# Performance work log

Hardware: AMD Instinct MI355X
Metric: run time of the kernel (lower is better)

Reference implementation:

```python
import jax, jax.numpy as jnp
import numpy as np

CLIP_LIMIT = 4.0
GRID = (8, 8)
NBINS = 256
B, H, W = 8, 2048, 2048


def setup_inputs() -> dict:
    key = jax.random.key(0)
    img = jax.random.randint(key, (B, H, W), 0, 256).astype(jnp.float32)
    return {"image": img}


def _clahe(image):
    b, h, w = image.shape
    gy, gx = GRID
    th, tw = h // gy, w // gx
    area = th * tw
    # quantize to bins (indices are non-differentiable constants)
    bins = jnp.clip(jax.lax.stop_gradient(image), 0, 255).astype(jnp.int32)  # [B,H,W]

    # ---- per-tile 256-bin histograms via scatter-add ----
    tiles = bins.reshape(b, gy, th, gx, tw).transpose(0, 1, 3, 2, 4)
    tiles = tiles.reshape(b * gy * gx, area)                       # [ntiles, area]
    n = b * gy * gx
    hist = jnp.zeros((n, NBINS), jnp.int32).at[jnp.arange(n)[:, None], tiles].add(1)

    # ---- clip and redistribute excess (OpenCV semantics) ----
    clip_lim = max(int(CLIP_LIMIT * area / NBINS), 1)
    clipped = jnp.minimum(hist, clip_lim)
    excess = (hist - clipped).sum(-1)                              # [ntiles]
    clipped = clipped + (excess // NBINS)[:, None]
    residual = excess % NBINS
    step = jnp.maximum(NBINS // jnp.maximum(residual, 1), 1)       # [ntiles]
    i = jnp.arange(NBINS)
    clipped = clipped + jnp.where(
        (residual[:, None] > 0) & (i[None, :] % step[:, None] == 0), 1, 0)

    # ---- CDF -> per-tile LUT ----
    cdf = jnp.cumsum(clipped, axis=-1)
    lut = jnp.clip(jnp.round(cdf.astype(jnp.float32) * (255.0 / area)), 0.0, 255.0)
    lut = lut.reshape(b, gy, gx, NBINS)                            # [B,gy,gx,256]

    # ---- bilinear interpolation between the 4 neighboring tile LUTs ----
    yf = jnp.arange(h, dtype=jnp.float32) / th - 0.5
    xf = jnp.arange(w, dtype=jnp.float32) / tw - 0.5
    y1f, x1f = jnp.floor(yf), jnp.floor(xf)
    ya, xa = yf - y1f, xf - x1f                                    # frac weights
    y1 = jnp.clip(y1f.astype(jnp.int32), 0, gy - 1)
    y2 = jnp.clip(y1f.astype(jnp.int32) + 1, 0, gy - 1)
    x1 = jnp.clip(x1f.astype(jnp.int32), 0, gx - 1)
    x2 = jnp.clip(x1f.astype(jnp.int32) + 1, 0, gx - 1)

    bi = jnp.arange(b)[:, None, None]        # [B,1,1]
    Y1, Y2 = y1[None, :, None], y2[None, :, None]   # [1,H,1]
    X1, X2 = x1[None, None, :], x2[None, None, :]   # [1,1,W]
    l11 = lut[bi, Y1, X1, bins]
    l12 = lut[bi, Y1, X2, bins]
    l21 = lut[bi, Y2, X1, bins]
    l22 = lut[bi, Y2, X2, bins]

    wy = ya[None, :, None]
    wx = xa[None, None, :]
    res = (l11 * (1 - wx) + l12 * wx) * (1 - wy) + (l21 * (1 - wx) + l22 * wx) * wy
    return jnp.clip(jnp.round(res), 0.0, 255.0)


def reference(image) -> jnp.ndarray:
    return _clahe(image)
```

## Files before the change

kernel.cpp:

```cpp
#include <hip/hip_runtime.h>

#define NB 256
#define CLIP_LIM 1024
#define TSTRIDE 11
#define HSTRIDE 264
#define NSUB 32
#define ROWS 4

typedef float f32x4 __attribute__((ext_vector_type(4)));

__global__ __launch_bounds__(1024) void clahe_hist_lut(const float* __restrict__ img,
                                                       float* __restrict__ lut,
                                                       unsigned int* __restrict__ bins) {
    const int t   = blockIdx.x;
    const int b   = t >> 6;
    const int ty  = (t >> 3) & 7;
    const int tx  = t & 7;
    const int tid = threadIdx.x;
    const int sub = ((tid >> 6) << 1) | (tid & 1);

    __shared__ int h[NSUB * HSTRIDE];
    __shared__ int c[NB];
    __shared__ int s_excess;

    #pragma unroll
    for (int k = 0; k < 9; ++k) {
        const int idx = tid + k * 1024;
        if (idx < NSUB * HSTRIDE) h[idx] = 0;
    }
    if (tid == 0) s_excess = 0;
    __syncthreads();

    const float* base = img + ((size_t)b << 22) + (size_t)(ty * 256) * 2048 + tx * 256;
    unsigned int* bbase = bins + ((size_t)b << 20) + ty * 131072 + tx * 64;
    int* hw = &h[sub * HSTRIDE];

    for (int i = tid; i < 16384; i += 1024) {
        const int r = i >> 6;
        const int q = i & 63;
        const f32x4 v = __builtin_nontemporal_load(
            reinterpret_cast<const f32x4*>(base + (size_t)r * 2048 + q * 4));
        const int b0 = (int)fminf(fmaxf(v.x, 0.f), 255.f);
        const int b1 = (int)fminf(fmaxf(v.y, 0.f), 255.f);
        const int b2 = (int)fminf(fmaxf(v.z, 0.f), 255.f);
        const int b3 = (int)fminf(fmaxf(v.w, 0.f), 255.f);
        atomicAdd(&hw[b0], 1);
        atomicAdd(&hw[b1], 1);
        atomicAdd(&hw[b2], 1);
        atomicAdd(&hw[b3], 1);
        bbase[r * 512 + q] = (unsigned)b0 | ((unsigned)b1 << 8) |
                             ((unsigned)b2 << 16) | ((unsigned)b3 << 24);
    }
    __syncthreads();

    int clipped = 0;
    if (tid < NB) {
        int sum = 0;
        #pragma unroll
        for (int w = 0; w < NSUB; ++w) sum += h[w * HSTRIDE + tid];
        clipped = min(sum, CLIP_LIM);
        atomicAdd(&s_excess, sum - clipped);
    }
    __syncthreads();

    if (tid < NB) {
        const int excess   = s_excess;
        const int add      = excess >> 8;
        const int residual = excess & 255;
        int step = 256 / (residual > 0 ? residual : 1);
        if (step < 1) step = 1;
        c[tid] = clipped + add + ((residual > 0 && (tid % step) == 0) ? 1 : 0);
    }
    __syncthreads();

    #pragma unroll
    for (int off = 1; off < NB; off <<= 1) {
        int v = 0;
        if (tid < NB && tid >= off) v = c[tid - off];
        __syncthreads();
        if (tid < NB) c[tid] += v;
        __syncthreads();
    }

    if (tid < NB) {
        float lv = rintf((float)c[tid] * (255.0f / 65536.0f));
        lut[t * NB + tid] = fminf(fmaxf(lv, 0.f), 255.f);
    }
}

__global__ __launch_bounds__(256) void clahe_apply(const unsigned int* __restrict__ bins,
                                                   const float* __restrict__ lut,
                                                   float* __restrict__ out) {
    const int bi  = blockIdx.x;
    const int b   = bi >> 9;
    const int y0  = (bi & 511) * ROWS;
    const int tid = threadIdx.x;

    __shared__ float T[ROWS * NB * TSTRIDE];

    {
        const float yf  = (float)y0 * (1.0f / 256.0f) - 0.5f;
        const float y1f = floorf(yf);
        const int y1 = min(max((int)y1f, 0), 7);
        const int y2 = min(max((int)y1f + 1, 0), 7);
        const float* lb = lut + ((size_t)b << 14);
        float la[8], lc[8];
        #pragma unroll
        for (int xc = 0; xc < 8; ++xc) {
            la[xc] = lb[(y1 * 8 + xc) * NB + tid];
            lc[xc] = lb[(y2 * 8 + xc) * NB + tid];
        }
        #pragma unroll
        for (int r = 0; r < ROWS; ++r) {
            const float yfr = (float)(y0 + r) * (1.0f / 256.0f) - 0.5f;
            const float ya  = yfr - floorf(yfr);
            float* Tr = &T[r * NB * TSTRIDE + tid * TSTRIDE];
            #pragma unroll
            for (int k = 0; k < 10; ++k) {
                const int kc = (k == 0) ? 0 : ((k - 1 > 7) ? 7 : k - 1);
                Tr[k] = la[kc] * (1.0f - ya) + lc[kc] * ya;
            }
        }
    }
    __syncthreads();

    const size_t imgbase = ((size_t)b << 22) + (size_t)y0 * 2048;
    #pragma unroll
    for (int it = 0; it < 2 * ROWS; ++it) {
        const int r = it >> 1;
        const int i = (it & 1) * 256 + tid;
        const size_t prow = imgbase + (size_t)r * 2048;
        const unsigned int w = bins[(prow >> 2) + i];
        const float* Tr = &T[r * NB * TSTRIDE];
        float res[4];
        #pragma unroll
        for (int j = 0; j < 4; ++j) {
            const int x    = i * 4 + j;
            const float xf = (float)x * (1.0f / 256.0f) - 0.5f;
            const float fl = floorf(xf);
            const float xa = xf - fl;
            const int s    = (int)fl + 1;
            const int bn   = (w >> (8 * j)) & 255;
            const float* p = &Tr[bn * TSTRIDE + s];
            const float a  = p[0];
            const float b2 = p[1];
            const float v  = a + (b2 - a) * xa;
            res[j] = fminf(fmaxf(rintf(v), 0.f), 255.f);
        }
        const f32x4 o = { res[0], res[1], res[2], res[3] };
        __builtin_nontemporal_store(o, reinterpret_cast<f32x4*>(out + prow + i * 4));
    }
}

extern "C" void kernel_launch(void* const* d_in, const int* in_sizes, int n_in,
                              void* d_out, int out_size, void* d_ws, size_t ws_size,
                              hipStream_t stream) {
    const float* img = (const float*)d_in[0];
    float* out = (float*)d_out;
    float* lut = (float*)d_ws;
    unsigned int* bins = (unsigned int*)((char*)d_ws + 512 * 1024);

    clahe_hist_lut<<<512, 1024, 0, stream>>>(img, lut, bins);
    clahe_apply<<<8 * (2048 / ROWS), 256, 0, stream>>>(bins, lut, out);
}
```

Before: 79.79 us.

## Fuse histogram and apply into one cooperative kernel with register-held bins

Replaces the two-kernel pipeline with a single cooperative kernel. Each block builds its tile histogram and LUT, then waits on a grid-wide sync. It then interpolates its own tile using bin codes kept in registers, so the packed bins never round-trip through global memory. Each block loads only the 3x3 neighbouring LUTs into shared memory. The costs are a grid barrier, 32 registers of bins per thread, and a requirement that all 512 blocks of 512 threads be co-resident, which fails on most hardware configurations. If the cooperative launch fails, it falls back to the old two-kernel path.

```diff
diff --git a/kernel.cpp b/kernel.cpp
--- a/kernel.cpp
+++ b/kernel.cpp
@@ -1,13 +1,149 @@
 #include <hip/hip_runtime.h>
+#include <hip/hip_cooperative_groups.h>
+
+namespace cg = cooperative_groups;
 
 #define NB 256
 #define CLIP_LIM 1024
-#define TSTRIDE 11
 #define HSTRIDE 264
-#define NSUB 32
-#define ROWS 4
+#define NSUB 16
+#define NTH 512
+#define PW 3
+#define PROW (NB*PW)
 
 typedef float f32x4 __attribute__((ext_vector_type(4)));
+
+__global__ __launch_bounds__(NTH, 4) void clahe_fused(const float* __restrict__ img,
+                                                      float* __restrict__ lut,
+                                                      float* __restrict__ out) {
+    const int t   = blockIdx.x;
+    const int b   = t >> 6;
+    const int ty  = (t >> 3) & 7;
+    const int tx  = t & 7;
+    const int tid = threadIdx.x;
+    const int sub = ((tid >> 6) << 1) | (tid & 1);
+
+    __shared__ int   h[NSUB * HSTRIDE];
+    __shared__ int   c[NB];
+    __shared__ int   s_excess;
+    __shared__ float P[3 * PROW];
+
+    #pragma unroll
+    for (int k = 0; k < 9; ++k) {
+        const int idx = tid + k * NTH;
+        if (idx < NSUB * HSTRIDE) h[idx] = 0;
+    }
+    if (tid == 0) s_excess = 0;
+    __syncthreads();
+
+    const size_t tbase = ((size_t)b << 22) + (size_t)(ty * 256) * 2048 + tx * 256;
+    const float* base = img + tbase;
+    int* hw = &h[sub * HSTRIDE];
+
+    unsigned int breg[32];
+    #pragma unroll
+    for (int k = 0; k < 32; ++k) {
+        const int i = tid + k * NTH;
+        const int r = i >> 6;
+        const int q = i & 63;
+        const f32x4 v = __builtin_nontemporal_load(
+            reinterpret_cast<const f32x4*>(base + (size_t)r * 2048 + q * 4));
+        const int b0 = (int)fminf(fmaxf(v.x, 0.f), 255.f);
+        const int b1 = (int)fminf(fmaxf(v.y, 0.f), 255.f);
+        const int b2 = (int)fminf(fmaxf(v.z, 0.f), 255.f);
+        const int b3 = (int)fminf(fmaxf(v.w, 0.f), 255.f);
+        atomicAdd(&hw[b0], 1);
+        atomicAdd(&hw[b1], 1);
+        atomicAdd(&hw[b2], 1);
+        atomicAdd(&hw[b3], 1);
+        breg[k] = (unsigned)b0 | ((unsigned)b1 << 8) | ((unsigned)b2 << 16) | ((unsigned)b3 << 24);
+    }
+    __syncthreads();
+
+    int clipped = 0;
+    if (tid < NB) {
+        int sum = 0;
+        #pragma unroll
+        for (int w = 0; w < NSUB; ++w) sum += h[w * HSTRIDE + tid];
+        clipped = min(sum, CLIP_LIM);
+        atomicAdd(&s_excess, sum - clipped);
+    }
+    __syncthreads();
+
+    if (tid < NB) {
+        const int excess   = s_excess;
+        const int add      = excess >> 8;
+        const int residual = excess & 255;
+        int step = 256 / (residual > 0 ? residual : 1);
+        if (step < 1) step = 1;
+        c[tid] = clipped + add + ((residual > 0 && (tid % step) == 0) ? 1 : 0);
+    }
+    __syncthreads();
+
+    #pragma unroll
+    for (int off = 1; off < NB; off <<= 1) {
+        int v = 0;
+        if (tid < NB && tid >= off) v = c[tid - off];
+        __syncthreads();
+        if (tid < NB) c[tid] += v;
+        __syncthreads();
+    }
+
+    if (tid < NB) {
+        float lv = rintf((float)c[tid] * (255.0f / 65536.0f));
+        lut[t * NB + tid] = fminf(fmaxf(lv, 0.f), 255.f);
+    }
+
+    __threadfence();
+    cg::this_grid().sync();
+
+    if (tid < NB) {
+        const float* lb = lut + ((size_t)b << 14);
+        #pragma unroll
+        for (int ry = 0; ry < 3; ++ry) {
+            const int rr = min(max(ty - 1 + ry, 0), 7);
+            #pragma unroll
+            for (int kx = 0; kx < 3; ++kx) {
+                const int cc = min(max(tx - 1 + kx, 0), 7);
+                P[ry * PROW + tid * PW + kx] = lb[(rr * 8 + cc) * NB + tid];
+            }
+        }
+    }
+    __syncthreads();
+
+    const int xl   = (tid & 63) * 4;
+    const int s_x  = (xl >= 128) ? 1 : 0;
+    const float xa0 = (float)((xl + 128) & 255);
+
+    float* outp = out + tbase;
+    #pragma unroll
+    for (int k = 0; k < 32; ++k) {
+        const int i  = tid + k * NTH;
+        const int r  = i >> 6;
+        const int sy = (r >= 128) ? 1 : 0;
+        const float ya = (float)((r + 128) & 255) * (1.0f / 256.0f);
+        const float* P0 = &P[sy * PROW];
+        const float* P1 = &P[(sy + 1) * PROW];
+        const unsigned int w = breg[k];
+        float res[4];
+        #pragma unroll
+        for (int j = 0; j < 4; ++j) {
+            const int bn  = (w >> (8 * j)) & 255;
+            const int idx = bn * 3 + s_x;
+            const float l11 = P0[idx];
+            const float l12 = P0[idx + 1];
+            const float l21 = P1[idx];
+            const float l22 = P1[idx + 1];
+            const float xa  = (xa0 + (float)j) * (1.0f / 256.0f);
+            const float top = l11 + (l12 - l11) * xa;
+            const float bot = l21 + (l22 - l21) * xa;
+            const float v   = top + (bot - top) * ya;
+            res[j] = fminf(fmaxf(rintf(v), 0.f), 255.f);
+        }
+        const f32x4 o = { res[0], res[1], res[2], res[3] };
+        __builtin_nontemporal_store(o, reinterpret_cast<f32x4*>(outp + (size_t)r * 2048 + xl));
+    }
+}
 
 __global__ __launch_bounds__(1024) void clahe_hist_lut(const float* __restrict__ img,
                                                        float* __restrict__ lut,
@@ -19,14 +155,14 @@
     const int tid = threadIdx.x;
     const int sub = ((tid >> 6) << 1) | (tid & 1);
 
-    __shared__ int h[NSUB * HSTRIDE];
+    __shared__ int h[32 * HSTRIDE];
     __shared__ int c[NB];
     __shared__ int s_excess;
 
     #pragma unroll
     for (int k = 0; k < 9; ++k) {
         const int idx = tid + k * 1024;
-        if (idx < NSUB * HSTRIDE) h[idx] = 0;
+        if (idx < 32 * HSTRIDE) h[idx] = 0;
     }
     if (tid == 0) s_excess = 0;
     __syncthreads();
@@ -57,7 +193,7 @@
     if (tid < NB) {
         int sum = 0;
         #pragma unroll
-        for (int w = 0; w < NSUB; ++w) sum += h[w * HSTRIDE + tid];
+        for (int w = 0; w < 32; ++w) sum += h[w * HSTRIDE + tid];
         clipped = min(sum, CLIP_LIM);
         atomicAdd(&s_excess, sum - clipped);
     }
@@ -88,15 +224,16 @@
     }
 }
 
+#define TSTRIDE 11
 __global__ __launch_bounds__(256) void clahe_apply(const unsigned int* __restrict__ bins,
                                                    const float* __restrict__ lut,
                                                    float* __restrict__ out) {
     const int bi  = blockIdx.x;
     const int b   = bi >> 9;
-    const int y0  = (bi & 511) * ROWS;
+    const int y0  = (bi & 511) * 4;
     const int tid = threadIdx.x;
 
-    __shared__ float T[ROWS * NB * TSTRIDE];
+    __shared__ float T[4 * NB * TSTRIDE];
 
     {
         const float yf  = (float)y0 * (1.0f / 256.0f) - 0.5f;
@@ -111,14 +248,14 @@
             lc[xc] = lb[(y2 * 8 + xc) * NB + tid];
         }
         #pragma unroll
-        for (int r = 0; r < ROWS; ++r) {
+        for (int r = 0; r < 4; ++r) {
             const float yfr = (float)(y0 + r) * (1.0f / 256.0f) - 0.5f;
             const float ya  = yfr - floorf(yfr);
             float* Tr = &T[r * NB * TSTRIDE + tid * TSTRIDE];
             #pragma unroll
-            for (int k = 0; k < 10; ++k) {
-                const int kc = (k == 0) ? 0 : ((k - 1 > 7) ? 7 : k - 1);
-                Tr[k] = la[kc] * (1.0f - ya) + lc[kc] * ya;
+            for (int kk = 0; kk < 10; ++kk) {
+                const int kc = (kk == 0) ? 0 : ((kk - 1 > 7) ? 7 : kk - 1);
+                Tr[kk] = la[kc] * (1.0f - ya) + lc[kc] * ya;
             }
         }
     }
@@ -126,7 +263,7 @@
 
     const size_t imgbase = ((size_t)b << 22) + (size_t)y0 * 2048;
     #pragma unroll
-    for (int it = 0; it < 2 * ROWS; ++it) {
+    for (int it = 0; it < 8; ++it) {
         const int r = it >> 1;
         const int i = (it & 1) * 256 + tid;
         const size_t prow = imgbase + (size_t)r * 2048;
@@ -160,6 +297,11 @@
     float* lut = (float*)d_ws;
     unsigned int* bins = (unsigned int*)((char*)d_ws + 512 * 1024);
 
-    clahe_hist_lut<<<512, 1024, 0, stream>>>(img, lut, bins);
-    clahe_apply<<<8 * (2048 / ROWS), 256, 0, stream>>>(bins, lut, out);
+    void* args[] = { (void*)&img, (void*)&lut, (void*)&out };
+    hipError_t err = hipLaunchCooperativeKernel((const void*)clahe_fused,
+                                                dim3(512), dim3(NTH), args, 0, stream);
+    if (err != hipSuccess) {
+        clahe_hist_lut<<<512, 1024, 0, stream>>>(img, lut, bins);
+        clahe_apply<<<8 * 512, 256, 0, stream>>>(bins, lut, out);
+    }
 }
```

Result: slower. 176.2 us (+120.8%).

## Pack adjacent tile LUT pairs into 16-bit fixed point and shrink apply rows

Applied to the files above, without the earlier changes.

The apply kernel now stores each pair of horizontally adjacent row-interpolated LUT values as two 16-bit fixed-point integers in one 32-bit word. One LDS read then fetches both interpolation endpoints, and the per-pixel x-coordinate math becomes integer shift and mask arithmetic. Rows per block drop from 4 to 2, which shrinks shared memory and doubles the grid. Both kernels gain occupancy hints in launch_bounds, and the histogram load becomes a normal cached load instead of a nontemporal one. Fixed-point scaling by 256 must keep rounding identical to the float reference; values of at most 255*256 fit in 16 bits.

```diff
diff --git a/kernel.cpp b/kernel.cpp
--- a/kernel.cpp
+++ b/kernel.cpp
@@ -2,16 +2,15 @@
 
 #define NB 256
 #define CLIP_LIM 1024
-#define TSTRIDE 11
 #define HSTRIDE 264
 #define NSUB 32
-#define ROWS 4
+#define PSTRIDE 9
 
 typedef float f32x4 __attribute__((ext_vector_type(4)));
 
-__global__ __launch_bounds__(1024) void clahe_hist_lut(const float* __restrict__ img,
-                                                       float* __restrict__ lut,
-                                                       unsigned int* __restrict__ bins) {
+__global__ __launch_bounds__(1024, 8) void clahe_hist_lut(const float* __restrict__ img,
+                                                          float* __restrict__ lut,
+                                                          unsigned int* __restrict__ bins) {
     const int t   = blockIdx.x;
     const int b   = t >> 6;
     const int ty  = (t >> 3) & 7;
@@ -38,8 +37,7 @@
     for (int i = tid; i < 16384; i += 1024) {
         const int r = i >> 6;
         const int q = i & 63;
-        const f32x4 v = __builtin_nontemporal_load(
-            reinterpret_cast<const f32x4*>(base + (size_t)r * 2048 + q * 4));
+        const f32x4 v = *reinterpret_cast<const f32x4*>(base + (size_t)r * 2048 + q * 4);
         const int b0 = (int)fminf(fmaxf(v.x, 0.f), 255.f);
         const int b1 = (int)fminf(fmaxf(v.y, 0.f), 255.f);
         const int b2 = (int)fminf(fmaxf(v.z, 0.f), 255.f);
@@ -88,15 +86,15 @@
     }
 }
 
-__global__ __launch_bounds__(256) void clahe_apply(const unsigned int* __restrict__ bins,
-                                                   const float* __restrict__ lut,
-                                                   float* __restrict__ out) {
+__global__ __launch_bounds__(256, 8) void clahe_apply(const unsigned int* __restrict__ bins,
+                                                      const float* __restrict__ lut,
+                                                      float* __restrict__ out) {
     const int bi  = blockIdx.x;
-    const int b   = bi >> 9;
-    const int y0  = (bi & 511) * ROWS;
+    const int b   = bi >> 10;
+    const int y0  = (bi & 1023) * 2;
     const int tid = threadIdx.x;
 
-    __shared__ float T[ROWS * NB * TSTRIDE];
+    __shared__ unsigned int T[2 * NB * PSTRIDE];
 
     {
         const float yf  = (float)y0 * (1.0f / 256.0f) - 0.5f;
@@ -111,41 +109,43 @@
             lc[xc] = lb[(y2 * 8 + xc) * NB + tid];
         }
         #pragma unroll
-        for (int r = 0; r < ROWS; ++r) {
-            const float yfr = (float)(y0 + r) * (1.0f / 256.0f) - 0.5f;
-            const float ya  = yfr - floorf(yfr);
-            float* Tr = &T[r * NB * TSTRIDE + tid * TSTRIDE];
+        for (int r = 0; r < 2; ++r) {
+            const float q = (float)((y0 + r + 128) & 255);
+            float tv[10];
             #pragma unroll
             for (int k = 0; k < 10; ++k) {
                 const int kc = (k == 0) ? 0 : ((k - 1 > 7) ? 7 : k - 1);
-                Tr[k] = la[kc] * (1.0f - ya) + lc[kc] * ya;
+                tv[k] = la[kc] * (256.0f - q) + lc[kc] * q;
             }
+            unsigned int* Tr = &T[r * NB * PSTRIDE + tid * PSTRIDE];
+            #pragma unroll
+            for (int s = 0; s < 9; ++s)
+                Tr[s] = (unsigned int)tv[s] | ((unsigned int)tv[s + 1] << 16);
         }
     }
     __syncthreads();
 
     const size_t imgbase = ((size_t)b << 22) + (size_t)y0 * 2048;
     #pragma unroll
-    for (int it = 0; it < 2 * ROWS; ++it) {
+    for (int it = 0; it < 4; ++it) {
         const int r = it >> 1;
         const int i = (it & 1) * 256 + tid;
         const size_t prow = imgbase + (size_t)r * 2048;
         const unsigned int w = bins[(prow >> 2) + i];
-        const float* Tr = &T[r * NB * TSTRIDE];
+        const unsigned int* Tr = &T[r * NB * PSTRIDE];
+        const int x   = i * 4;
+        const int s   = (x + 128) >> 8;
+        const float xa0 = (float)((x + 128) & 255);
         float res[4];
         #pragma unroll
         for (int j = 0; j < 4; ++j) {
-            const int x    = i * 4 + j;
-            const float xf = (float)x * (1.0f / 256.0f) - 0.5f;
-            const float fl = floorf(xf);
-            const float xa = xf - fl;
-            const int s    = (int)fl + 1;
-            const int bn   = (w >> (8 * j)) & 255;
-            const float* p = &Tr[bn * TSTRIDE + s];
-            const float a  = p[0];
-            const float b2 = p[1];
-            const float v  = a + (b2 - a) * xa;
-            res[j] = fminf(fmaxf(rintf(v), 0.f), 255.f);
+            const int bn = (w >> (8 * j)) & 255;
+            const unsigned int u = Tr[bn * PSTRIDE + s];
+            const float a  = (float)(u & 0xFFFFu);
+            const float bb = (float)(u >> 16);
+            const float xa = (xa0 + (float)j) * (1.0f / 256.0f);
+            const float v  = a + (bb - a) * xa;
+            res[j] = fminf(fmaxf(rintf(v * (1.0f / 256.0f)), 0.f), 255.f);
         }
         const f32x4 o = { res[0], res[1], res[2], res[3] };
         __builtin_nontemporal_store(o, reinterpret_cast<f32x4*>(out + prow + i * 4));
@@ -161,5 +161,5 @@
     unsigned int* bins = (unsigned int*)((char*)d_ws + 512 * 1024);
 
     clahe_hist_lut<<<512, 1024, 0, stream>>>(img, lut, bins);
-    clahe_apply<<<8 * (2048 / ROWS), 256, 0, stream>>>(bins, lut, out);
+    clahe_apply<<<8 * 1024, 256, 0, stream>>>(bins, lut, out);
 }
```

Measured after the change: 78.33 us. About the same (-1.8%).
